# Kernel tuning notes

Hardware: AMD Instinct MI355X
Metric: run time of the kernel (lower is better)

Reference implementation:

```python
import jax, jax.numpy as jnp
import numpy as np

TOKENS, DIM, N_EXPERTS, TOPK = 8192, 4096, 256, 8

def setup_inputs() -> dict:
    key = jax.random.key(0)
    k1, k2 = jax.random.split(key)
    x = jax.random.normal(k1, (TOKENS, DIM), dtype=jnp.float32)
    weight = jax.random.normal(k2, (N_EXPERTS, DIM), dtype=jnp.float32) * (DIM ** -0.5)
    return {"x": x, "weight": weight}

def reference(x, weight):
    # logits: [tokens, n_experts]
    logits = jnp.einsum('td,ed->te', x, weight)
    scores = jax.nn.sigmoid(logits)
    topv, indices = jax.lax.top_k(scores, TOPK)          # [tokens, topk]
    gates = topv / jnp.sum(topv, axis=-1, keepdims=True)
    return gates, indices
```

## Files before the change

kernel.cpp:

```cpp
#include <hip/hip_runtime.h>
#include <hip/hip_bf16.h>
#include <hip/hip_fp16.h>
#include <math.h>

#define TOKENS   8192
#define DIM      4096
#define NEXP     256
#define TOPK     8
#define CAND     12

#define MT3      128
#define BK3      64
#define KG       (DIM / 32)

typedef _Float16 f16x8 __attribute__((ext_vector_type(8)));
typedef _Float16 f16x4 __attribute__((ext_vector_type(4)));
typedef float    f32x4 __attribute__((ext_vector_type(4)));

typedef const __attribute__((address_space(1))) unsigned int* gas_ptr;
typedef       __attribute__((address_space(3))) unsigned int* las_ptr;

__global__ __launch_bounds__(256)
void convert_w(const float* __restrict__ w, _Float16* __restrict__ whs) {
    const int g = blockIdx.x * 256 + threadIdx.x;
    const int tile = g >> 6, c = g & 63;
    const int q = c >> 4, r = c & 15;
    const int ng = tile / KG, kg = tile % KG;
    const int n = ng * 16 + r, k = kg * 32 + q * 8;
    const float4 a = *(const float4*)(w + (size_t)n * DIM + k);
    const float4 b = *(const float4*)(w + (size_t)n * DIM + k + 4);
    f16x8 h;
    h[0] = (_Float16)a.x; h[1] = (_Float16)a.y;
    h[2] = (_Float16)a.z; h[3] = (_Float16)a.w;
    h[4] = (_Float16)b.x; h[5] = (_Float16)b.y;
    h[6] = (_Float16)b.z; h[7] = (_Float16)b.w;
    *(f16x8*)(whs + (size_t)g * 8) = h;
}

__global__ __launch_bounds__(512, 2)
void gemm_v3(const float* __restrict__ x, const _Float16* __restrict__ whs,
             float* __restrict__ logits, int kspan) {
    __shared__ _Float16 As[16 * 512];
    __shared__ _Float16 Bs[32 * 512];

    const int t = threadIdx.x, w = t >> 6, lane = t & 63;
    const int m0 = blockIdx.x * MT3;
    const int kb = blockIdx.y * kspan;
    float* lp    = logits + (size_t)blockIdx.y * TOKENS * NEXP;

    const int rg = w >> 2;
    const int cg = w & 3;

    const int am  = t >> 2;
    const int ack = (t & 3) * 2;
    const int amg = am >> 4, amr = am & 15;
    const int aoff0 = ((amg * 2 + (ack >> 2)) * 64 + (ack & 3) * 16 + amr) * 8;
    const int ack1  = ack + 1;
    const int aoff1 = ((amg * 2 + (ack1 >> 2)) * 64 + (ack1 & 3) * 16 + amr) * 8;

    f32x4 acc[4][4];
    #pragma unroll
    for (int i = 0; i < 4; ++i)
        #pragma unroll
        for (int j = 0; j < 4; ++j) acc[i][j] = (f32x4){0.f, 0.f, 0.f, 0.f};

    const float* xrow = x + (size_t)(m0 + am) * DIM + ack * 8;
    float4 xr0 = *(const float4*)(xrow + kb);
    float4 xr1 = *(const float4*)(xrow + kb + 4);
    float4 xr2 = *(const float4*)(xrow + kb + 8);
    float4 xr3 = *(const float4*)(xrow + kb + 12);

    for (int k0 = kb; k0 < kb + kspan; k0 += BK3) {
        #pragma unroll
        for (int c = 0; c < 4; ++c) {
            const int ti  = w * 4 + c;
            const int ng  = ti >> 1, kgl = ti & 1;
            const _Float16* gp = whs + ((size_t)(ng * KG + (k0 >> 5) + kgl)) * 512
                                     + lane * 8;
            __builtin_amdgcn_global_load_lds((gas_ptr)gp, (las_ptr)&Bs[ti * 512],
                                             16, 0, 0);
        }
        {
            f16x8 h0, h1;
            h0[0] = (_Float16)xr0.x; h0[1] = (_Float16)xr0.y;
            h0[2] = (_Float16)xr0.z; h0[3] = (_Float16)xr0.w;
            h0[4] = (_Float16)xr1.x; h0[5] = (_Float16)xr1.y;
            h0[6] = (_Float16)xr1.z; h0[7] = (_Float16)xr1.w;
            h1[0] = (_Float16)xr2.x; h1[1] = (_Float16)xr2.y;
            h1[2] = (_Float16)xr2.z; h1[3] = (_Float16)xr2.w;
            h1[4] = (_Float16)xr3.x; h1[5] = (_Float16)xr3.y;
            h1[6] = (_Float16)xr3.z; h1[7] = (_Float16)xr3.w;
            *(f16x8*)&As[aoff0] = h0;
            *(f16x8*)&As[aoff1] = h1;
        }
        __syncthreads();

        if (k0 + BK3 < kb + kspan) {
            xr0 = *(const float4*)(xrow + k0 + BK3);
            xr1 = *(const float4*)(xrow + k0 + BK3 + 4);
            xr2 = *(const float4*)(xrow + k0 + BK3 + 8);
            xr3 = *(const float4*)(xrow + k0 + BK3 + 12);
        }

        #pragma unroll
        for (int kk = 0; kk < 2; ++kk) {
            f16x8 af[4], bf[4];
            #pragma unroll
            for (int mt = 0; mt < 4; ++mt)
                af[mt] = *(const f16x8*)&As[(((rg * 4 + mt) * 2 + kk) * 64 + lane) * 8];
            #pragma unroll
            for (int nt = 0; nt < 4; ++nt)
                bf[nt] = *(const f16x8*)&Bs[(((cg * 4 + nt) * 2 + kk) * 64 + lane) * 8];
            #pragma unroll
            for (int mt = 0; mt < 4; ++mt)
                #pragma unroll
                for (int nt = 0; nt < 4; ++nt)
                    acc[mt][nt] = __builtin_amdgcn_mfma_f32_16x16x32_f16(
                        af[mt], bf[nt], acc[mt][nt], 0, 0, 0);
        }
        __syncthreads();
    }

    #pragma unroll
    for (int mt = 0; mt < 4; ++mt) {
        #pragma unroll
        for (int nt = 0; nt < 4; ++nt) {
            #pragma unroll
            for (int r = 0; r < 4; ++r) {
                const int m = m0 + (rg * 4 + mt) * 16 + (lane >> 4) * 4 + r;
                const int n = (cg * 4 + nt) * 16 + (lane & 15);
                lp[(size_t)m * NEXP + n] = acc[mt][nt][r];
            }
        }
    }
}

__global__ __launch_bounds__(256)
void topk_cand(const float* __restrict__ logits, int* __restrict__ cand,
               int nsplit) {
    const int lane  = threadIdx.x & 63;
    const int token = blockIdx.x * 4 + (threadIdx.x >> 6);
    const float* lp = logits + (size_t)token * NEXP;

    float s[4];
    #pragma unroll
    for (int j = 0; j < 4; ++j) s[j] = 0.f;
    for (int p = 0; p < nsplit; ++p) {
        const float* pp = lp + (size_t)p * TOKENS * NEXP;
        #pragma unroll
        for (int j = 0; j < 4; ++j) s[j] += pp[j * 64 + lane];
    }

    int mye = 0;
    #pragma unroll
    for (int r = 0; r < CAND; ++r) {
        float bv = s[0];
        int   be = lane;
        #pragma unroll
        for (int j = 1; j < 4; ++j) {
            if (s[j] > bv) { bv = s[j]; be = j * 64 + lane; }
        }
        #pragma unroll
        for (int off = 32; off > 0; off >>= 1) {
            const float ov = __shfl_xor(bv, off, 64);
            const int   oe = __shfl_xor(be, off, 64);
            if (ov > bv || (ov == bv && oe < be)) { bv = ov; be = oe; }
        }
        if (lane == r) mye = be;
        if ((be & 63) == lane) s[be >> 6] = -1e30f;
    }

    if (lane < CAND) cand[token * CAND + lane] = mye;
}

__global__ __launch_bounds__(256)
void rescore(const float* __restrict__ x, const float* __restrict__ w,
             const int* __restrict__ cand, float* __restrict__ out) {
    const int wave = threadIdx.x >> 6, lane = threadIdx.x & 63;
    const int token = blockIdx.x * 4 + wave;

    const float4* xp4 = (const float4*)(x + (size_t)token * DIM);

    int ce[CAND];
    const float4* wp[CAND];
    #pragma unroll
    for (int c = 0; c < CAND; ++c) {
        ce[c] = __builtin_amdgcn_readfirstlane(cand[token * CAND + c]);
        wp[c] = (const float4*)(w + (size_t)ce[c] * DIM);
    }

    double acc[2 * CAND];
    #pragma unroll
    for (int c = 0; c < 2 * CAND; ++c) acc[c] = 0.0;

    #pragma unroll 2
    for (int i = 0; i < 16; ++i) {
        const int o = lane + i * 64;
        const float4 xv = xp4[o];
        const double dx = (double)xv.x, dy = (double)xv.y;
        const double dz = (double)xv.z, dw = (double)xv.w;
        #pragma unroll
        for (int c = 0; c < CAND; ++c) {
            const float4 wv = wp[c][o];
            double e = fma(dx, (double)wv.x, acc[2 * c]);
            acc[2 * c] = fma(dy, (double)wv.y, e);
            double f = fma(dz, (double)wv.z, acc[2 * c + 1]);
            acc[2 * c + 1] = fma(dw, (double)wv.w, f);
        }
    }

    double tot[CAND];
    #pragma unroll
    for (int c = 0; c < CAND; ++c) tot[c] = acc[2 * c] + acc[2 * c + 1];

    #pragma unroll
    for (int off = 32; off > 0; off >>= 1) {
        #pragma unroll
        for (int c = 0; c < CAND; ++c)
            tot[c] += __shfl_xor(tot[c], off, 64);
    }

    int rank[CAND];
    #pragma unroll
    for (int c = 0; c < CAND; ++c) {
        int r = 0;
        #pragma unroll
        for (int j = 0; j < CAND; ++j) {
            if (j == c) continue;
            if (tot[j] > tot[c] || (tot[j] == tot[c] && ce[j] < ce[c])) ++r;
        }
        rank[c] = r;
    }

    float sig[CAND];
    float sum = 0.f;
    #pragma unroll
    for (int c = 0; c < CAND; ++c) {
        sig[c] = 1.0f / (1.0f + expf(-(float)tot[c]));
        if (rank[c] < TOPK) sum += sig[c];
    }

    if (lane < TOPK) {
        float g = 0.f; int ei = 0;
        #pragma unroll
        for (int c = 0; c < CAND; ++c)
            if (rank[c] == lane) { g = sig[c]; ei = ce[c]; }
        out[(size_t)token * TOPK + lane] = g / sum;
        out[(size_t)TOKENS * TOPK + (size_t)token * TOPK + lane] = (float)ei;
    }
}

extern "C" void kernel_launch(void* const* d_in, const int* in_sizes, int n_in,
                              void* d_out, int out_size, void* d_ws, size_t ws_size,
                              hipStream_t stream) {
    const float* x = (const float*)d_in[0];
    const float* w = (const float*)d_in[1];
    float* out     = (float*)d_out;

    const size_t plane = (size_t)TOKENS * NEXP * sizeof(float);
    const size_t fixed = (size_t)TOKENS * CAND * sizeof(int)
                       + (size_t)NEXP * DIM * sizeof(_Float16);
    int S = 4;
    if (ws_size < 4 * plane + fixed) S = (ws_size >= 2 * plane + fixed) ? 2 : 1;

    float*     logits = (float*)d_ws;
    int*       candp  = (int*)((char*)d_ws + (size_t)S * plane);
    _Float16*  whs    = (_Float16*)((char*)candp + (size_t)TOKENS * CAND * sizeof(int));

    convert_w<<<512, 256, 0, stream>>>(w, whs);
    dim3 ggrid(TOKENS / MT3, S);
    gemm_v3<<<ggrid, 512, 0, stream>>>(x, whs, logits, DIM / S);
    topk_cand<<<TOKENS / 4, 256, 0, stream>>>(logits, candp, S);
    rescore<<<TOKENS / 4, 256, 0, stream>>>(x, w, candp, out);
}
```

Before: 358.4 us.

## Shrink GEMM tile to 64 rows with 256-thread blocks and prefetch rescore loads

The logits GEMM now uses 64-token tiles with 4 waves, each wave covering all 64 rows and a 64-expert slice. This doubles the grid and targets 3 blocks per CU instead of 2, at the cost of loading the full B tile per block for half as many rows. The fp64 rescore loop now double-buffers its x and candidate weight loads in registers, so the next iteration's loads are issued before the current FMAs. That prefetch raises register pressure with 24 float4 buffers.

```diff
diff --git a/kernel.cpp b/kernel.cpp
--- a/kernel.cpp
+++ b/kernel.cpp
@@ -9,12 +9,11 @@
 #define TOPK     8
 #define CAND     12
 
-#define MT3      128
+#define MT4      64
 #define BK3      64
 #define KG       (DIM / 32)
 
 typedef _Float16 f16x8 __attribute__((ext_vector_type(8)));
-typedef _Float16 f16x4 __attribute__((ext_vector_type(4)));
 typedef float    f32x4 __attribute__((ext_vector_type(4)));
 
 typedef const __attribute__((address_space(1))) unsigned int* gas_ptr;
@@ -37,19 +36,16 @@
     *(f16x8*)(whs + (size_t)g * 8) = h;
 }
 
-__global__ __launch_bounds__(512, 2)
-void gemm_v3(const float* __restrict__ x, const _Float16* __restrict__ whs,
+__global__ __launch_bounds__(256, 3)
+void gemm_v4(const float* __restrict__ x, const _Float16* __restrict__ whs,
              float* __restrict__ logits, int kspan) {
-    __shared__ _Float16 As[16 * 512];
+    __shared__ _Float16 As[8 * 512];
     __shared__ _Float16 Bs[32 * 512];
 
     const int t = threadIdx.x, w = t >> 6, lane = t & 63;
-    const int m0 = blockIdx.x * MT3;
+    const int m0 = blockIdx.x * MT4;
     const int kb = blockIdx.y * kspan;
     float* lp    = logits + (size_t)blockIdx.y * TOKENS * NEXP;
-
-    const int rg = w >> 2;
-    const int cg = w & 3;
 
     const int am  = t >> 2;
     const int ack = (t & 3) * 2;
@@ -72,8 +68,8 @@
 
     for (int k0 = kb; k0 < kb + kspan; k0 += BK3) {
         #pragma unroll
-        for (int c = 0; c < 4; ++c) {
-            const int ti  = w * 4 + c;
+        for (int c = 0; c < 8; ++c) {
+            const int ti  = w * 8 + c;
             const int ng  = ti >> 1, kgl = ti & 1;
             const _Float16* gp = whs + ((size_t)(ng * KG + (k0 >> 5) + kgl)) * 512
                                      + lane * 8;
@@ -107,10 +103,10 @@
             f16x8 af[4], bf[4];
             #pragma unroll
             for (int mt = 0; mt < 4; ++mt)
-                af[mt] = *(const f16x8*)&As[(((rg * 4 + mt) * 2 + kk) * 64 + lane) * 8];
+                af[mt] = *(const f16x8*)&As[((mt * 2 + kk) * 64 + lane) * 8];
             #pragma unroll
             for (int nt = 0; nt < 4; ++nt)
-                bf[nt] = *(const f16x8*)&Bs[(((cg * 4 + nt) * 2 + kk) * 64 + lane) * 8];
+                bf[nt] = *(const f16x8*)&Bs[(((w * 4 + nt) * 2 + kk) * 64 + lane) * 8];
             #pragma unroll
             for (int mt = 0; mt < 4; ++mt)
                 #pragma unroll
@@ -127,8 +123,8 @@
         for (int nt = 0; nt < 4; ++nt) {
             #pragma unroll
             for (int r = 0; r < 4; ++r) {
-                const int m = m0 + (rg * 4 + mt) * 16 + (lane >> 4) * 4 + r;
-                const int n = (cg * 4 + nt) * 16 + (lane & 15);
+                const int m = m0 + mt * 16 + (lane >> 4) * 4 + r;
+                const int n = (w * 4 + nt) * 16 + (lane & 15);
                 lp[(size_t)m * NEXP + n] = acc[mt][nt][r];
             }
         }
@@ -193,19 +189,27 @@
     #pragma unroll
     for (int c = 0; c < 2 * CAND; ++c) acc[c] = 0.0;
 
-    #pragma unroll 2
+    float4 xb[2], wb[2][CAND];
+    xb[0] = xp4[lane];
+    #pragma unroll
+    for (int c = 0; c < CAND; ++c) wb[0][c] = wp[c][lane];
+
+    #pragma unroll
     for (int i = 0; i < 16; ++i) {
-        const int o = lane + i * 64;
-        const float4 xv = xp4[o];
-        const double dx = (double)xv.x, dy = (double)xv.y;
-        const double dz = (double)xv.z, dw = (double)xv.w;
+        const int cur = i & 1, nxt = cur ^ 1;
+        if (i < 15) {
+            const int o = lane + (i + 1) * 64;
+            xb[nxt] = xp4[o];
+            #pragma unroll
+            for (int c = 0; c < CAND; ++c) wb[nxt][c] = wp[c][o];
+        }
+        const double dx = (double)xb[cur].x, dy = (double)xb[cur].y;
+        const double dz = (double)xb[cur].z, dw = (double)xb[cur].w;
         #pragma unroll
         for (int c = 0; c < CAND; ++c) {
-            const float4 wv = wp[c][o];
-            double e = fma(dx, (double)wv.x, acc[2 * c]);
-            acc[2 * c] = fma(dy, (double)wv.y, e);
-            double f = fma(dz, (double)wv.z, acc[2 * c + 1]);
-            acc[2 * c + 1] = fma(dw, (double)wv.w, f);
+            const float4 wv = wb[cur][c];
+            acc[2 * c]     = fma(dy, (double)wv.y, fma(dx, (double)wv.x, acc[2 * c]));
+            acc[2 * c + 1] = fma(dw, (double)wv.w, fma(dz, (double)wv.z, acc[2 * c + 1]));
         }
     }
 
@@ -268,8 +272,8 @@
     _Float16*  whs    = (_Float16*)((char*)candp + (size_t)TOKENS * CAND * sizeof(int));
 
     convert_w<<<512, 256, 0, stream>>>(w, whs);
-    dim3 ggrid(TOKENS / MT3, S);
-    gemm_v3<<<ggrid, 512, 0, stream>>>(x, whs, logits, DIM / S);
+    dim3 ggrid(TOKENS / MT4, S);
+    gemm_v4<<<ggrid, 256, 0, stream>>>(x, whs, logits, DIM / S);
     topk_cand<<<TOKENS / 4, 256, 0, stream>>>(logits, candp, S);
     rescore<<<TOKENS / 4, 256, 0, stream>>>(x, w, candp, out);
 }
```

New measurement: 318.7 us. 1.12x faster.
